# Kernel optimization log

Hardware: AMD Instinct MI355X
Metric: run time of the kernel (lower is better)

Reference implementation:

```python
import jax, jax.numpy as jnp
import numpy as np

B2 = 8192  # 2 * batch (two SimCLR views)
D = 512    # feature_dim


def setup_inputs() -> dict:
    key = jax.random.key(0)
    k1, k2, k3 = jax.random.split(key, 3)
    feature = jax.random.normal(k1, (B2, D), dtype=jnp.float32)
    # sigma (diagonal variances) must be strictly positive: uniform in [0.5, 1.5]
    sigma_v = jax.random.uniform(k2, (B2, D), dtype=jnp.float32, minval=0.5, maxval=1.5)
    # label indexes the (B2-1) skip-self columns -> values in [0, B2-2]
    label = jax.random.randint(k3, (B2,), 0, B2 - 1)
    return {"feature": feature, "sigma_v": sigma_v, "label": label}


def reference(feature, sigma_v, label):
    n, d = feature.shape
    rows = jnp.arange(n)
    cols = jnp.arange(n - 1)
    # gather_index[b, k] = k if k < b else k + 1  (all indices except b)
    gi = cols[None, :] + (cols[None, :] >= rows[:, None]).astype(jnp.int32)  # (B2, B2-1)

    inv_s = 1.0 / sigma_v
    # weighted Mahalanobis: dist[i, j] = sum_d (x_i - x_j)^2 / sigma_j, expanded to GEMMs
    t1 = (feature * feature) @ inv_s.T                 # sum_d x_i^2 / sigma_j
    t2 = feature @ (feature * inv_s).T                 # sum_d x_i x_j / sigma_j
    t3 = jnp.sum(feature * feature * inv_s, axis=1)    # sum_d x_j^2 / sigma_j
    dist = t1 - 2.0 * t2 + t3[None, :]                 # (B2, B2)

    dist_g = jnp.take_along_axis(dist, gi, axis=1)               # (B2, B2-1)
    gt = jnp.take_along_axis(dist_g, label[:, None], axis=1)     # (B2, 1)
    logit = jnp.exp(0.1 * (gt - dist_g))                         # (B2, B2-1)

    # absolute index of each row's positive sample
    pos_idx = jnp.take_along_axis(gi, label[:, None], axis=1)[:, 0]  # (B2,)
    # ratio[i, j] = prod_d sqrt(sigma_i[d] / sigma_pos(j)[d]) = exp(0.5 * (ls[i] - ls[pos(j)]))
    ls = jnp.sum(jnp.log(sigma_v), axis=1)                           # (B2,)
    ratio_g = jnp.exp(0.5 * (ls[:, None] - ls[pos_idx][gi]))         # (B2, B2-1)

    logit_mat = ratio_g * logit
    loss = jnp.mean(jnp.log(jnp.sum(logit_mat, axis=1)))
    return loss, logit_mat
```

## Files before the change

kernel.cpp:

```cpp
#include <hip/hip_runtime.h>
#include <hip/hip_bf16.h>
#include <stdint.h>

#define B2 8192
#define D  512
#define K2 1024
#define NM1 (B2 - 1)
#define NT  16

typedef _Float16 f16;
typedef _Float16 f16x2 __attribute__((ext_vector_type(2)));
typedef _Float16 f16x8 __attribute__((ext_vector_type(8)));
typedef float    f32x4 __attribute__((ext_vector_type(4)));

__global__ __launch_bounds__(256) void prep(
    const float* __restrict__ feat, const float* __restrict__ sig,
    const int* __restrict__ label,
    f16* __restrict__ Ahat, f16* __restrict__ Bhat,
    float* __restrict__ rowc, float* __restrict__ colc2, float* __restrict__ rowsum)
{
    int i = blockIdx.x;
    int t = threadIdx.x;
    int lb = label[i];
    int p  = lb + (lb >= i ? 1 : 0);

    const float2 xv  = ((const float2*)(feat + (size_t)i * D))[t];
    const float2 sv  = ((const float2*)(sig  + (size_t)i * D))[t];
    const float2 xpv = ((const float2*)(feat + (size_t)p * D))[t];
    const float2 spv = ((const float2*)(sig  + (size_t)p * D))[t];

    float inv0 = 1.0f / sv.x, inv1 = 1.0f / sv.y;
    float x20 = xv.x * xv.x, x21 = xv.y * xv.y;

    f16* Ar = Ahat + (size_t)i * K2;
    f16* Br = Bhat + (size_t)i * K2;
    *(f16x2*)&Ar[2 * t]       = f16x2{(f16)x20, (f16)x21};
    *(f16x2*)&Ar[512 + 2 * t] = f16x2{(f16)xv.x, (f16)xv.y};
    *(f16x2*)&Br[2 * t]       = f16x2{(f16)inv0, (f16)inv1};
    *(f16x2*)&Br[512 + 2 * t] = f16x2{(f16)(-2.0f * xv.x * inv0), (f16)(-2.0f * xv.y * inv1)};

    float t3p = x20 * inv0 + x21 * inv1;
    float lsp = __logf(sv.x) + __logf(sv.y);
    float lpp = __logf(spv.x) + __logf(spv.y);
    float dx0 = xv.x - xpv.x, dx1 = xv.y - xpv.y;
    float gtp = dx0 * dx0 / spv.x + dx1 * dx1 / spv.y;

    for (int off = 32; off; off >>= 1) {
        t3p += __shfl_down(t3p, off);
        lsp += __shfl_down(lsp, off);
        lpp += __shfl_down(lpp, off);
        gtp += __shfl_down(gtp, off);
    }
    __shared__ float w0[4], w1[4], w2[4], w3[4];
    int lane = t & 63, w = t >> 6;
    if (lane == 0) { w0[w] = t3p; w1[w] = lsp; w2[w] = lpp; w3[w] = gtp; }
    __syncthreads();
    if (t == 0) {
        float t3 = w0[0] + w0[1] + w0[2] + w0[3];
        float ls = w1[0] + w1[1] + w1[2] + w1[3];
        float lp = w2[0] + w2[1] + w2[2] + w2[3];
        float gt = w3[0] + w3[1] + w3[2] + w3[3];
        rowc[i]  = 0.1f * gt + 0.5f * ls;
        colc2[i] = -0.5f * lp - 0.1f * t3;
        rowsum[i] = 0.0f;
    }
}


#define GLDS16(src, dst)                                                       \
  __builtin_amdgcn_global_load_lds(                                            \
      (const __attribute__((address_space(1))) unsigned int*)(src),            \
      (__attribute__((address_space(3))) unsigned int*)(dst), 16, 0, 0)

#define STAGE_HALF(gbase, hrow, koff, dstbase)                                 \
  do {                                                                         \
    GLDS16((gbase) + (size_t)(hrow) * K2 + (koff), (dstbase) + w512);          \
    GLDS16((gbase) + (size_t)((hrow) + 64) * K2 + (koff),                      \
           (dstbase) + 4096 + w512);                                           \
  } while (0)

template <int VM>
__device__ __forceinline__ void kquad(
    const f16* Asb, const f16* Bsb,
    f16* AsN,
    f16* BsC,
    const f16* gA, const f16* gB, int w512,
    int doA, int kA, int doB, int kB,
    int wr128, int wc64, int l15, int lhi, int l7,
    f32x4 (&acc)[8][4])
{
    f16x8 bf[4][2], af[2][2];

    #pragma unroll
    for (int ni = 0; ni < 4; ++ni)
        #pragma unroll
        for (int ks = 0; ks < 2; ++ks)
            bf[ni][ks] = *(const f16x8*)&Bsb[(wc64 + ni * 16 + l15) * 64 +
                                             (((ks * 4 + lhi) ^ l7) * 8)];
    #pragma unroll
    for (int m = 0; m < 2; ++m)
        #pragma unroll
        for (int ks = 0; ks < 2; ++ks)
            af[m][ks] = *(const f16x8*)&Asb[(wr128 + m * 16 + l15) * 64 +
                                            (((ks * 4 + lhi) ^ l7) * 8)];
    if (doA) { STAGE_HALF(gA, 0, kA, AsN); }
    asm volatile("" ::: "memory");
    __builtin_amdgcn_s_barrier();
    asm volatile("s_waitcnt lgkmcnt(0)" ::: "memory");
    __builtin_amdgcn_sched_barrier(0);
    __builtin_amdgcn_s_setprio(1);
    #pragma unroll
    for (int m = 0; m < 2; ++m)
        #pragma unroll
        for (int ni = 0; ni < 4; ++ni)
            #pragma unroll
            for (int ks = 0; ks < 2; ++ks)
                acc[m][ni] = __builtin_amdgcn_mfma_f32_16x16x32_f16(
                    af[m][ks], bf[ni][ks], acc[m][ni], 0, 0, 0);
    __builtin_amdgcn_s_setprio(0);
    __builtin_amdgcn_s_barrier();

    #pragma unroll
    for (int m = 0; m < 2; ++m)
        #pragma unroll
        for (int ks = 0; ks < 2; ++ks)
            af[m][ks] = *(const f16x8*)&Asb[(wr128 + (2 + m) * 16 + l15) * 64 +
                                            (((ks * 4 + lhi) ^ l7) * 8)];
    if (doA) { STAGE_HALF(gA, 128, kA, AsN + 8192); }
    asm volatile("" ::: "memory");
    if (doB) { STAGE_HALF(gB, 0, kB, BsC); }
    asm volatile("" ::: "memory");
    __builtin_amdgcn_s_barrier();
    asm volatile("s_waitcnt lgkmcnt(0)" ::: "memory");
    __builtin_amdgcn_sched_barrier(0);
    __builtin_amdgcn_s_setprio(1);
    #pragma unroll
    for (int m = 0; m < 2; ++m)
        #pragma unroll
        for (int ni = 0; ni < 4; ++ni)
            #pragma unroll
            for (int ks = 0; ks < 2; ++ks)
                acc[2 + m][ni] = __builtin_amdgcn_mfma_f32_16x16x32_f16(
                    af[m][ks], bf[ni][ks], acc[2 + m][ni], 0, 0, 0);
    __builtin_amdgcn_s_setprio(0);
    __builtin_amdgcn_s_barrier();

    #pragma unroll
    for (int m = 0; m < 2; ++m)
        #pragma unroll
        for (int ks = 0; ks < 2; ++ks)
            af[m][ks] = *(const f16x8*)&Asb[(wr128 + (4 + m) * 16 + l15) * 64 +
                                            (((ks * 4 + lhi) ^ l7) * 8)];
    if (doB) { STAGE_HALF(gB, 128, kB, BsC + 8192); }
    asm volatile("" ::: "memory");
    __builtin_amdgcn_s_barrier();
    asm volatile("s_waitcnt lgkmcnt(0)" ::: "memory");
    __builtin_amdgcn_sched_barrier(0);
    __builtin_amdgcn_s_setprio(1);
    #pragma unroll
    for (int m = 0; m < 2; ++m)
        #pragma unroll
        for (int ni = 0; ni < 4; ++ni)
            #pragma unroll
            for (int ks = 0; ks < 2; ++ks)
                acc[4 + m][ni] = __builtin_amdgcn_mfma_f32_16x16x32_f16(
                    af[m][ks], bf[ni][ks], acc[4 + m][ni], 0, 0, 0);
    __builtin_amdgcn_s_setprio(0);
    __builtin_amdgcn_s_barrier();

    #pragma unroll
    for (int m = 0; m < 2; ++m)
        #pragma unroll
        for (int ks = 0; ks < 2; ++ks)
            af[m][ks] = *(const f16x8*)&Asb[(wr128 + (6 + m) * 16 + l15) * 64 +
                                            (((ks * 4 + lhi) ^ l7) * 8)];
    __builtin_amdgcn_s_barrier();
    asm volatile("s_waitcnt lgkmcnt(0)" ::: "memory");
    __builtin_amdgcn_sched_barrier(0);
    __builtin_amdgcn_s_setprio(1);
    #pragma unroll
    for (int m = 0; m < 2; ++m)
        #pragma unroll
        for (int ni = 0; ni < 4; ++ni)
            #pragma unroll
            for (int ks = 0; ks < 2; ++ks)
                acc[6 + m][ni] = __builtin_amdgcn_mfma_f32_16x16x32_f16(
                    af[m][ks], bf[ni][ks], acc[6 + m][ni], 0, 0, 0);
    __builtin_amdgcn_s_setprio(0);
    if (VM == 4) asm volatile("s_waitcnt vmcnt(4)" ::: "memory");
    else         asm volatile("s_waitcnt vmcnt(0)" ::: "memory");
    __builtin_amdgcn_s_barrier();
}

__global__ __launch_bounds__(512, 1) void gemm_epilogue(
    const f16* __restrict__ Ahat, const f16* __restrict__ Bhat,
    const float* __restrict__ rowc, const float* __restrict__ colc2,
    float* __restrict__ rowsum, float* __restrict__ out)
{
    __shared__ f16 As[2][256 * 64];
    __shared__ f16 Bs[2][256 * 64];
    __shared__ float rS[256], cS[256];

    int bid = blockIdx.x;
    int rr = bid >> 3, x = bid & 7;
    int bm = x * 4 + (rr & 3);
    int bn = rr >> 2;

    int t = threadIdx.x;
    int l = t & 63, w = t >> 6;
    int wr128 = (w >> 2) * 128;
    int wc64  = (w & 3) * 64;
    int l15 = l & 15, lhi = l >> 4, l7 = l & 7;
    int w512 = w * 512;

    int gcs = (t & 7) ^ ((t >> 3) & 7);
    const f16* gA = Ahat + (size_t)(bm * 256 + (t >> 3)) * K2 + gcs * 8;
    const f16* gB = Bhat + (size_t)(bn * 256 + (t >> 3)) * K2 + gcs * 8;

    if (t < 256) rS[t]       = rowc[bm * 256 + t];
    else         cS[t - 256] = colc2[bn * 256 + (t - 256)];

    STAGE_HALF(gA, 0,   0,  &As[0][0]);
    STAGE_HALF(gA, 128, 0,  &As[0][8192]);
    STAGE_HALF(gB, 0,   0,  &Bs[0][0]);
    STAGE_HALF(gB, 128, 0,  &Bs[0][8192]);
    STAGE_HALF(gB, 0,   64, &Bs[1][0]);
    STAGE_HALF(gB, 128, 64, &Bs[1][8192]);
    __syncthreads();

    f32x4 acc[8][4];
    #pragma unroll
    for (int a = 0; a < 8; ++a)
        #pragma unroll
        for (int b = 0; b < 4; ++b) acc[a][b] = f32x4{0.f, 0.f, 0.f, 0.f};

    #pragma unroll 1
    for (int it = 0; it < 7; ++it) {
        int T = 2 * it;
        kquad<4>(&As[0][0], &Bs[0][0], &As[1][0], &Bs[0][0], gA, gB, w512,
                 1, (T + 1) * 64, 1, (T + 2) * 64,
                 wr128, wc64, l15, lhi, l7, acc);
        kquad<4>(&As[1][0], &Bs[1][0], &As[0][0], &Bs[1][0], gA, gB, w512,
                 1, (T + 2) * 64, 1, (T + 3) * 64,
                 wr128, wc64, l15, lhi, l7, acc);
    }
    kquad<0>(&As[0][0], &Bs[0][0], &As[1][0], &Bs[0][0], gA, gB, w512,
             1, 15 * 64, 0, 0, wr128, wc64, l15, lhi, l7, acc);
    kquad<0>(&As[1][0], &Bs[1][0], &As[0][0], &Bs[1][0], gA, gB, w512,
             0, 0, 0, 0, wr128, wc64, l15, lhi, l7, acc);

    int qd = l >> 4, lc = l & 15;
    #pragma unroll
    for (int mi = 0; mi < 8; ++mi) {
        #pragma unroll
        for (int rg = 0; rg < 4; ++rg) {
            int il = wr128 + mi * 16 + qd * 4 + rg;
            int i  = bm * 256 + il;
            float rc = rS[il];
            float part = 0.f;
            #pragma unroll
            for (int ni = 0; ni < 4; ++ni) {
                int jl = wc64 + ni * 16 + lc;
                int j  = bn * 256 + jl;
                float v = __expf(rc - 0.1f * acc[mi][ni][rg] + cS[jl]);
                if (j != i) {
                    out[1 + (size_t)i * NM1 + (j - (j > i ? 1 : 0))] = v;
                    part += v;
                }
            }
            part += __shfl_xor(part, 1);
            part += __shfl_xor(part, 2);
            part += __shfl_xor(part, 4);
            part += __shfl_xor(part, 8);
            if (lc == 0) atomicAdd(&rowsum[i], part);
        }
    }
}

__global__ __launch_bounds__(256) void loss_k(const float* __restrict__ rowsum,
                                              float* __restrict__ out)
{
    int t = threadIdx.x;
    float s = 0.f;
    for (int r = t; r < B2; r += 256) s += __logf(rowsum[r]);
    for (int off = 32; off; off >>= 1) s += __shfl_down(s, off);
    __shared__ float wv[4];
    if ((t & 63) == 0) wv[t >> 6] = s;
    __syncthreads();
    if (t == 0) out[0] = (wv[0] + wv[1] + wv[2] + wv[3]) * (1.0f / (float)B2);
}

extern "C" void kernel_launch(void* const* d_in, const int* in_sizes, int n_in,
                              void* d_out, int out_size, void* d_ws, size_t ws_size,
                              hipStream_t stream) {
    const float* feat  = (const float*)d_in[0];
    const float* sig   = (const float*)d_in[1];
    const int*   label = (const int*)d_in[2];
    float* out = (float*)d_out;

    char* ws = (char*)d_ws;
    f16* Ahat = (f16*)ws;
    f16* Bhat = (f16*)(ws + (size_t)B2 * K2 * 2);
    float* rowc   = (float*)(ws + (size_t)B2 * K2 * 4);
    float* colc2  = rowc + B2;
    float* rowsum = colc2 + B2;

    prep<<<dim3(B2), dim3(256), 0, stream>>>(feat, sig, label, Ahat, Bhat, rowc, colc2, rowsum);
    gemm_epilogue<<<dim3(1024), dim3(512), 0, stream>>>(Ahat, Bhat, rowc, colc2, rowsum, out);
    loss_k<<<dim3(1), dim3(256), 0, stream>>>(rowsum, out);
}
```

Measured before the change: 463.1 us.

## Restage A tile in row-slices to refill buffers early and relax waits

```diff
diff --git a/kernel.cpp b/kernel.cpp
--- a/kernel.cpp
+++ b/kernel.cpp
@@ -6,7 +6,6 @@
 #define D  512
 #define K2 1024
 #define NM1 (B2 - 1)
-#define NT  16
 
 typedef _Float16 f16;
 typedef _Float16 f16x2 __attribute__((ext_vector_type(2)));
@@ -79,13 +78,18 @@
            (dstbase) + 4096 + w512);                                           \
   } while (0)
 
+#define STAGE_ASLICE(gAslice, s, kk, dstbase)                                  \
+  GLDS16((gAslice) + (size_t)(s) * 32 * K2 + (kk),                             \
+         (dstbase) + (size_t)(wbase + 32 * (s)) * 64)
+
 template <int VM>
 __device__ __forceinline__ void kquad(
     const f16* Asb, const f16* Bsb,
-    f16* AsN,
-    f16* BsC,
-    const f16* gA, const f16* gB, int w512,
-    int doA, int kA, int doB, int kB,
+    f16* AsP,
+    f16* AsC, f16* BsC,
+    const f16* gAs, const f16* gB, int w512, int wbase,
+    int doA3, int kA1,
+    int doN,  int kN,
     int wr128, int wc64, int l15, int lhi, int l7,
     f32x4 (&acc)[8][4])
 {
@@ -103,7 +107,7 @@
         for (int ks = 0; ks < 2; ++ks)
             af[m][ks] = *(const f16x8*)&Asb[(wr128 + m * 16 + l15) * 64 +
                                             (((ks * 4 + lhi) ^ l7) * 8)];
-    if (doA) { STAGE_HALF(gA, 0, kA, AsN); }
+    if (doA3) { STAGE_ASLICE(gAs, 3, kA1, AsP); }
     asm volatile("" ::: "memory");
     __builtin_amdgcn_s_barrier();
     asm volatile("s_waitcnt lgkmcnt(0)" ::: "memory");
@@ -126,9 +130,10 @@
         for (int ks = 0; ks < 2; ++ks)
             af[m][ks] = *(const f16x8*)&Asb[(wr128 + (2 + m) * 16 + l15) * 64 +
                                             (((ks * 4 + lhi) ^ l7) * 8)];
-    if (doA) { STAGE_HALF(gA, 128, kA, AsN + 8192); }
-    asm volatile("" ::: "memory");
-    if (doB) { STAGE_HALF(gB, 0, kB, BsC); }
+    if (doN) {
+        STAGE_ASLICE(gAs, 0, kN, AsC);
+        STAGE_HALF(gB, 0, kN, BsC);
+    }
     asm volatile("" ::: "memory");
     __builtin_amdgcn_s_barrier();
     asm volatile("s_waitcnt lgkmcnt(0)" ::: "memory");
@@ -151,7 +156,10 @@
         for (int ks = 0; ks < 2; ++ks)
             af[m][ks] = *(const f16x8*)&Asb[(wr128 + (4 + m) * 16 + l15) * 64 +
                                             (((ks * 4 + lhi) ^ l7) * 8)];
-    if (doB) { STAGE_HALF(gB, 128, kB, BsC + 8192); }
+    if (doN) {
+        STAGE_ASLICE(gAs, 1, kN, AsC);
+        STAGE_HALF(gB, 128, kN, BsC + 8192);
+    }
     asm volatile("" ::: "memory");
     __builtin_amdgcn_s_barrier();
     asm volatile("s_waitcnt lgkmcnt(0)" ::: "memory");
@@ -174,6 +182,8 @@
         for (int ks = 0; ks < 2; ++ks)
             af[m][ks] = *(const f16x8*)&Asb[(wr128 + (6 + m) * 16 + l15) * 64 +
                                             (((ks * 4 + lhi) ^ l7) * 8)];
+    if (doN) { STAGE_ASLICE(gAs, 2, kN, AsC); }
+    asm volatile("" ::: "memory");
     __builtin_amdgcn_s_barrier();
     asm volatile("s_waitcnt lgkmcnt(0)" ::: "memory");
     __builtin_amdgcn_sched_barrier(0);
@@ -187,8 +197,8 @@
                 acc[6 + m][ni] = __builtin_amdgcn_mfma_f32_16x16x32_f16(
                     af[m][ks], bf[ni][ks], acc[6 + m][ni], 0, 0, 0);
     __builtin_amdgcn_s_setprio(0);
-    if (VM == 4) asm volatile("s_waitcnt vmcnt(4)" ::: "memory");
-    else         asm volatile("s_waitcnt vmcnt(0)" ::: "memory");
+    if (VM == 7)      asm volatile("s_waitcnt vmcnt(7)" ::: "memory");
+    else if (VM == 0) asm volatile("s_waitcnt vmcnt(0)" ::: "memory");
     __builtin_amdgcn_s_barrier();
 }
 
@@ -212,10 +222,13 @@
     int wc64  = (w & 3) * 64;
     int l15 = l & 15, lhi = l >> 4, l7 = l & 7;
     int w512 = w * 512;
+    int wbase = 8 * w + (w >= 4 ? 96 : 0);
 
     int gcs = (t & 7) ^ ((t >> 3) & 7);
     const f16* gA = Ahat + (size_t)(bm * 256 + (t >> 3)) * K2 + gcs * 8;
     const f16* gB = Bhat + (size_t)(bn * 256 + (t >> 3)) * K2 + gcs * 8;
+    int grow0 = (t >> 3) + ((t >> 3) >= 32 ? 96 : 0);
+    const f16* gAs = Ahat + (size_t)(bm * 256 + grow0) * K2 + gcs * 8;
 
     if (t < 256) rS[t]       = rowc[bm * 256 + t];
     else         cS[t - 256] = colc2[bn * 256 + (t - 256)];
@@ -226,6 +239,9 @@
     STAGE_HALF(gB, 128, 0,  &Bs[0][8192]);
     STAGE_HALF(gB, 0,   64, &Bs[1][0]);
     STAGE_HALF(gB, 128, 64, &Bs[1][8192]);
+    STAGE_ASLICE(gAs, 0, 64, &As[1][0]);
+    STAGE_ASLICE(gAs, 1, 64, &As[1][0]);
+    STAGE_ASLICE(gAs, 2, 64, &As[1][0]);
     __syncthreads();
 
     f32x4 acc[8][4];
@@ -237,17 +253,19 @@
     #pragma unroll 1
     for (int it = 0; it < 7; ++it) {
         int T = 2 * it;
-        kquad<4>(&As[0][0], &Bs[0][0], &As[1][0], &Bs[0][0], gA, gB, w512,
-                 1, (T + 1) * 64, 1, (T + 2) * 64,
+        kquad<7>(&As[0][0], &Bs[0][0], &As[1][0], &As[0][0], &Bs[0][0],
+                 gAs, gB, w512, wbase, 1, (T + 1) * 64, 1, (T + 2) * 64,
                  wr128, wc64, l15, lhi, l7, acc);
-        kquad<4>(&As[1][0], &Bs[1][0], &As[0][0], &Bs[1][0], gA, gB, w512,
-                 1, (T + 2) * 64, 1, (T + 3) * 64,
+        kquad<7>(&As[1][0], &Bs[1][0], &As[0][0], &As[1][0], &Bs[1][0],
+                 gAs, gB, w512, wbase, 1, (T + 2) * 64, 1, (T + 3) * 64,
                  wr128, wc64, l15, lhi, l7, acc);
     }
-    kquad<0>(&As[0][0], &Bs[0][0], &As[1][0], &Bs[0][0], gA, gB, w512,
-             1, 15 * 64, 0, 0, wr128, wc64, l15, lhi, l7, acc);
-    kquad<0>(&As[1][0], &Bs[1][0], &As[0][0], &Bs[1][0], gA, gB, w512,
-             0, 0, 0, 0, wr128, wc64, l15, lhi, l7, acc);
+    kquad<0>(&As[0][0], &Bs[0][0], &As[1][0], &As[0][0], &Bs[0][0],
+             gAs, gB, w512, wbase, 1, 15 * 64, 0, 0,
+             wr128, wc64, l15, lhi, l7, acc);
+    kquad<-1>(&As[1][0], &Bs[1][0], &As[0][0], &As[1][0], &Bs[1][0],
+              gAs, gB, w512, wbase, 0, 0, 0, 0,
+              wr128, wc64, l15, lhi, l7, acc);
 
     int qd = l >> 4, lc = l & 15;
     #pragma unroll
```

Result: faster. 447.0 us (-3.5%).
